# Performance work log

Hardware: AMD Instinct MI355X
Metric: run time of the kernel (lower is better)

## Reference

```python
import jax, jax.numpy as jnp
import numpy as np

N_NODES = 32000
N_EDGES = 320000
N_GRAPHS = 1600
HID = 128
RBF = 32
ZDIM = 2 * HID + RBF  # CGConv concat dim = 288


def setup_inputs() -> dict:
    key = jax.random.key(0)
    ks = jax.random.split(key, 20)
    inp = {
        "x": jax.random.randint(ks[0], (N_NODES,), 0, 100),
        "edge_index": jax.random.randint(ks[1], (2, N_EDGES), 0, N_NODES),
        "edge_attr": jax.random.normal(ks[2], (N_EDGES, RBF), dtype=jnp.float32),
        "batch": jnp.sort(jax.random.randint(ks[3], (N_NODES,), 0, N_GRAPHS)),
        "emb": jax.random.normal(ks[4], (100, HID), dtype=jnp.float32) * 0.02,
    }
    s = 1.0 / np.sqrt(ZDIM)
    for i, k0 in zip((1, 2, 3), range(5, 11, 2)):
        inp[f"Wf{i}"] = jax.random.uniform(ks[k0], (ZDIM, HID), jnp.float32, -s, s)
        inp[f"bf{i}"] = jnp.zeros((HID,), jnp.float32)
        inp[f"Ws{i}"] = jax.random.uniform(ks[k0 + 1], (ZDIM, HID), jnp.float32, -s, s)
        inp[f"bs{i}"] = jnp.zeros((HID,), jnp.float32)
    sl = 1.0 / np.sqrt(HID)
    inp["Wlin"] = jax.random.uniform(ks[11], (HID, HID), jnp.float32, -sl, sl)
    inp["blin"] = jnp.zeros((HID,), jnp.float32)
    return inp


def _cgconv(h, src, dst, ea, Wf, bf, Ws, bs):
    # PyG CGConv: z = [x_i, x_j, e_ij]; msg = sigmoid(lin_f(z)) * softplus(lin_s(z)); out = x + sum_j msg
    z = jnp.concatenate([h[dst], h[src], ea], axis=1)  # [E, 288]
    msg = jax.nn.sigmoid(z @ Wf + bf) * jax.nn.softplus(z @ Ws + bs)  # [E, 128]
    return h + jax.ops.segment_sum(msg, dst, num_segments=N_NODES)


def reference(x, edge_index, edge_attr, batch, emb,
              Wf1, bf1, Ws1, bs1, Wf2, bf2, Ws2, bs2, Wf3, bf3, Ws3, bs3,
              Wlin, blin):
    src, dst = edge_index[0], edge_index[1]
    h = emb[x]  # [N, 128] embedding lookup
    h = jax.nn.relu(_cgconv(h, src, dst, edge_attr, Wf1, bf1, Ws1, bs1))
    h = jax.nn.relu(_cgconv(h, src, dst, edge_attr, Wf2, bf2, Ws2, bs2))
    h = jax.nn.relu(_cgconv(h, src, dst, edge_attr, Wf3, bf3, Ws3, bs3))
    # global mean pool over graphs
    sums = jax.ops.segment_sum(h, batch, num_segments=N_GRAPHS)  # [G, 128]
    cnt = jax.ops.segment_sum(jnp.ones((N_NODES,), h.dtype), batch, num_segments=N_GRAPHS)
    pooled = sums / jnp.maximum(cnt, 1.0)[:, None]
    return pooled @ Wlin + blin  # [G, 128]
```

## Files before the change

### kernel.cpp

```cpp
#include <hip/hip_runtime.h>
#include <math.h>

#define NN 32000
#define NE 320000
#define NG 1600

using frag_ab = __attribute__((ext_vector_type(8))) short;
using frag_cd = __attribute__((ext_vector_type(4))) float;
typedef float v2f __attribute__((ext_vector_type(2)));

static __device__ __forceinline__ unsigned short f2bf(float f) {
  unsigned u = __builtin_bit_cast(unsigned, f);
  unsigned r = u + 0x7fff + ((u >> 16) & 1);
  return (unsigned short)(r >> 16);
}
static __device__ __forceinline__ float bflo(unsigned u) {
  return __builtin_bit_cast(float, u << 16);
}
static __device__ __forceinline__ float bfhi(unsigned u) {
  return __builtin_bit_cast(float, u & 0xffff0000u);
}
static __device__ __forceinline__ v2f unpk(unsigned u) {
  return (v2f){bflo(u), bfhi(u)};
}

__global__ __launch_bounds__(256) void k_misc(const int* __restrict__ x,
                                              const float* __restrict__ emb,
                                              const float* __restrict__ Wf1, const float* __restrict__ Ws1,
                                              const float* __restrict__ Wf2, const float* __restrict__ Ws2,
                                              const float* __restrict__ Wf3, const float* __restrict__ Ws3,
                                              float* __restrict__ h,
                                              unsigned short* __restrict__ hb,
                                              unsigned short* __restrict__ accumb,
                                              unsigned short* __restrict__ wedge,
                                              unsigned short* __restrict__ wgemm) {
  int b = blockIdx.x;
  int tid = threadIdx.x;
  if (b < 2000) {
    int idx = b * 256 + tid;
    int n = idx >> 4;
    int c8 = (idx & 15) << 3;
    const float* e = emb + (size_t)x[n] * 128 + c8;
    float4 v0 = *(const float4*)e;
    float4 v1 = *(const float4*)(e + 4);
    float* hp = h + (size_t)n * 128 + c8;
    *(float4*)hp = v0;
    *(float4*)(hp + 4) = v1;
    ushort4 p0, p1;
    p0.x = f2bf(v0.x); p0.y = f2bf(v0.y); p0.z = f2bf(v0.z); p0.w = f2bf(v0.w);
    p1.x = f2bf(v1.x); p1.y = f2bf(v1.y); p1.z = f2bf(v1.z); p1.w = f2bf(v1.w);
    unsigned short* hbp = hb + (size_t)n * 128 + c8;
    *(ushort4*)hbp = p0;
    *(ushort4*)(hbp + 4) = p1;
    *(uint4*)(accumb + (size_t)n * 128 + c8) = make_uint4(0, 0, 0, 0);
  } else if (b < 2096) {
    int idx = (b - 2000) * 256 + tid;
    int l = idx >> 13;
    int r = idx & 8191;
    int cc = r >> 5;
    int k = r & 31;
    int w = cc >> 6, t = (cc >> 4) & 3, c = cc & 15;
    const float* Wf = (l == 0) ? Wf1 : (l == 1) ? Wf2 : Wf3;
    const float* Ws = (l == 0) ? Ws1 : (l == 1) ? Ws2 : Ws3;
    const float* W = (t < 2) ? Wf : Ws;
    int ch = w * 32 + 2 * c + (t & 1);
    wedge[(size_t)l * 8192 + cc * 32 + k] = f2bf(W[(size_t)(256 + k) * 128 + ch]);
  } else {
    int idx = (b - 2096) * 256 + tid;
    int l = idx >> 16;
    int r = idx & 65535;
    int cc = r >> 7;
    int k = r & 127;
    int p = (cc & ~31) + ((cc & 15) << 1) + ((cc >> 4) & 1);
    int ph = p & 255;
    int j = ph >> 2, sub = ph & 3;
    const float* Wf = (l == 0) ? Wf1 : (l == 1) ? Wf2 : Wf3;
    const float* Ws = (l == 0) ? Ws1 : (l == 1) ? Ws2 : Ws3;
    const float* W = (sub < 2) ? Wf : Ws;
    int ch = 2 * j + (sub & 1);
    int krow = ((p < 256) ? 0 : 128) + k;
    wgemm[(size_t)l * 65536 + cc * 128 + k] = f2bf(W[(size_t)krow * 128 + ch]);
  }
}

__global__ __launch_bounds__(256) void k_histb(const int* __restrict__ ei,
                                               const int* __restrict__ batch,
                                               int* __restrict__ counts,
                                               int* __restrict__ starts) {
  int b = blockIdx.x;
  int tid = threadIdx.x;
  if (b < 1250) {
    int e = b * 256 + tid;
    atomicAdd(counts + ei[NE + e], 1);
  } else {
    int n = (b - 1250) * 256 + tid;
    if (n > NN) return;
    if (n == NN) {
      starts[NG] = NN;
      int last = batch[NN - 1];
      for (int g = last + 1; g < NG; ++g) starts[g] = NN;
    } else if (n == 0) {
      int bb = batch[0];
      for (int g = 0; g <= bb; ++g) starts[g] = 0;
    } else {
      int b0 = batch[n - 1], b1 = batch[n];
      for (int g = b0 + 1; g <= b1; ++g) starts[g] = n;
    }
  }
}

__global__ __launch_bounds__(1024) void k_scan(const int* __restrict__ counts,
                                               int* __restrict__ offs) {
  __shared__ int part[1024];
  __shared__ int carry_s;
  int t = threadIdx.x;
  if (t == 0) carry_s = 0;
  __syncthreads();
  for (int chunk = 0; chunk < 4; ++chunk) {
    int base = chunk * 8192 + t * 8;
    int4 a = make_int4(0, 0, 0, 0), bq = make_int4(0, 0, 0, 0);
    bool full = (base + 8 <= NN);
    if (full) {
      a = *(const int4*)(counts + base);
      bq = *(const int4*)(counts + base + 4);
    }
    int e1 = a.x, e2 = e1 + a.y, e3 = e2 + a.z, e4 = e3 + a.w;
    int e5 = e4 + bq.x, e6 = e5 + bq.y, e7 = e6 + bq.z;
    int run = e7 + bq.w;
    part[t] = run;
    __syncthreads();
    for (int off = 1; off < 1024; off <<= 1) {
      int v = (t >= off) ? part[t - off] : 0;
      __syncthreads();
      part[t] += v;
      __syncthreads();
    }
    int excl = carry_s + ((t == 0) ? 0 : part[t - 1]);
    if (full) {
      int4 o0 = make_int4(excl, excl + e1, excl + e2, excl + e3);
      int4 o1 = make_int4(excl + e4, excl + e5, excl + e6, excl + e7);
      *(int4*)(offs + base) = o0;
      *(int4*)(offs + base + 4) = o1;
    }
    __syncthreads();
    if (t == 0) carry_s += part[1023];
    __syncthreads();
  }
}

__global__ __launch_bounds__(256) void k_scat1(const int* __restrict__ ei,
                                               int* __restrict__ offs,
                                               int* __restrict__ perm) {
  int e = blockIdx.x * 256 + threadIdx.x;
  int d = ei[NE + e];
  int pos = atomicAdd(offs + d, 1);
  perm[pos] = e;
}

__global__ __launch_bounds__(256) void k_scat2(const int* __restrict__ ei,
                                               const float* __restrict__ ea,
                                               const int* __restrict__ perm,
                                               int* __restrict__ srcp,
                                               int* __restrict__ dstp,
                                               unsigned short* __restrict__ eab) {
  __shared__ int se[64];
  int b = blockIdx.x;
  int t = threadIdx.x;
  int base = b * 64;
  if (t < 64) {
    int e = perm[base + t];
    se[t] = e;
    srcp[base + t] = ei[e];
    dstp[base + t] = ei[NE + e];
  }
  __syncthreads();
  int x = t >> 2;
  int ck = t & 3;
  int e = se[x];
  const float* a = ea + (size_t)e * 32 + ck * 8;
  float4 v0 = *(const float4*)a;
  float4 v1 = *(const float4*)(a + 4);
  int p = (((x >> 2) & 3) << 4) | ((x >> 4) << 2) | (x & 3);
  unsigned short* q = eab + (size_t)(base + p) * 32 + ck * 8;
  ushort4 o0, o1;
  o0.x = f2bf(v0.x); o0.y = f2bf(v0.y); o0.z = f2bf(v0.z); o0.w = f2bf(v0.w);
  o1.x = f2bf(v1.x); o1.y = f2bf(v1.y); o1.z = f2bf(v1.z); o1.w = f2bf(v1.w);
  *(ushort4*)q = o0;
  *(ushort4*)(q + 4) = o1;
}

__global__ __launch_bounds__(256) void k_gemm(const unsigned short* __restrict__ hb,
                                              const unsigned short* __restrict__ wgemmL,
                                              unsigned short* __restrict__ T) {
  __shared__ short sA[64 * 136];
  __shared__ short sB[128 * 136];
  int m0 = blockIdx.x * 64;
  int n0 = blockIdx.y * 128;
  int tid = threadIdx.x;
#pragma unroll
  for (int i = 0; i < 4; ++i) {
    int idx = tid + i * 256;
    int row = idx >> 4, chk = idx & 15;
    uint4 v = *(const uint4*)(hb + (size_t)(m0 + row) * 128 + chk * 8);
    *(uint4*)&sA[row * 136 + chk * 8] = v;
  }
#pragma unroll
  for (int i = 0; i < 8; ++i) {
    int idx = tid + i * 256;
    int col = idx >> 4, chk = idx & 15;
    uint4 v = *(const uint4*)(wgemmL + (size_t)(n0 + col) * 128 + chk * 8);
    *(uint4*)&sB[col * 136 + chk * 8] = v;
  }
  __syncthreads();
  int w = tid >> 6, lane = tid & 63, c = lane & 15, q = lane >> 4;
  frag_cd acc[4][2];
#pragma unroll
  for (int mt = 0; mt < 4; ++mt)
#pragma unroll
    for (int t = 0; t < 2; ++t) acc[mt][t] = (frag_cd){0.f, 0.f, 0.f, 0.f};
#pragma unroll
  for (int ks = 0; ks < 4; ++ks) {
    frag_ab Af[4], Bf[2];
#pragma unroll
    for (int mt = 0; mt < 4; ++mt)
      Af[mt] = *(const frag_ab*)&sA[(mt * 16 + c) * 136 + ks * 32 + q * 8];
#pragma unroll
    for (int t = 0; t < 2; ++t)
      Bf[t] = *(const frag_ab*)&sB[(w * 32 + t * 16 + c) * 136 + ks * 32 + q * 8];
#pragma unroll
    for (int mt = 0; mt < 4; ++mt)
#pragma unroll
      for (int t = 0; t < 2; ++t)
        acc[mt][t] = __builtin_amdgcn_mfma_f32_16x16x32_bf16(Af[mt], Bf[t], acc[mt][t], 0, 0, 0);
  }
  int nbase = n0 + w * 32 + 2 * c;
#pragma unroll
  for (int mt = 0; mt < 4; ++mt) {
#pragma unroll
    for (int r = 0; r < 4; ++r) {
      int node = m0 + mt * 16 + q * 4 + r;
      unsigned pk = (unsigned)f2bf(acc[mt][0][r]) | ((unsigned)f2bf(acc[mt][1][r]) << 16);
      *(unsigned*)(T + (size_t)node * 512 + nbase) = pk;
    }
  }
}

__global__ __launch_bounds__(256) void k_edge(const int* __restrict__ srcp,
                                              const int* __restrict__ dstp,
                                              const unsigned short* __restrict__ eab,
                                              const unsigned short* __restrict__ T,
                                              const unsigned short* __restrict__ wedgeL,
                                              const float* __restrict__ bf,
                                              const float* __restrict__ bs,
                                              unsigned short* __restrict__ accumb) {
  __shared__ short sA[64 * 40];
  __shared__ short sB[256 * 40];
  __shared__ float sbf[128], sbs[128];
  __shared__ int sSrc[64], sDst[64];
  int tid = threadIdx.x;
  int e0 = blockIdx.x * 64;
  {
    int row = tid >> 2, qq = tid & 3;
    uint4 v = *(const uint4*)(eab + (size_t)e0 * 32 + tid * 8);
    *(uint4*)&sA[row * 40 + qq * 8] = v;
  }
#pragma unroll
  for (int i = 0; i < 4; ++i) {
    int idx = tid + i * 256;
    int col = idx >> 2, qq = idx & 3;
    uint4 v = *(const uint4*)(wedgeL + (size_t)col * 32 + qq * 8);
    *(uint4*)&sB[col * 40 + qq * 8] = v;
  }
  if (tid < 128) {
    sbf[tid] = bf[tid];
    sbs[tid] = bs[tid];
  } else if (tid < 192) {
    sSrc[tid - 128] = srcp[e0 + tid - 128] * 512 + 256;
  } else {
    sDst[tid - 192] = dstp[e0 + tid - 192] * 512;
  }
  __syncthreads();

  int w = tid >> 6;
  int lane = tid & 63;
  int c = lane & 15;
  int q = lane >> 4;

  frag_ab Af[4], Bf[4];
#pragma unroll
  for (int et = 0; et < 4; ++et)
    Af[et] = *(const frag_ab*)&sA[(et * 16 + c) * 40 + q * 8];
#pragma unroll
  for (int t = 0; t < 4; ++t)
    Bf[t] = *(const frag_ab*)&sB[(w * 64 + t * 16 + c) * 40 + q * 8];

  frag_cd acc[4][4];
#pragma unroll
  for (int et = 0; et < 4; ++et)
#pragma unroll
    for (int t = 0; t < 4; ++t)
      acc[et][t] = (frag_cd){0.f, 0.f, 0.f, 0.f};
#pragma unroll
  for (int et = 0; et < 4; ++et)
#pragma unroll
    for (int t = 0; t < 4; ++t)
      acc[et][t] = __builtin_amdgcn_mfma_f32_16x16x32_bf16(Af[et], Bf[t], acc[et][t], 0, 0, 0);

  int ch = w * 32 + 2 * c;
  int jo = ch * 2;
  v2f bfv = {sbf[ch], sbf[ch + 1]};
  v2f bsv = {sbs[ch], sbs[ch + 1]};

  int prevd = sDst[q * 16];
  v2f av = {0.f, 0.f};
#pragma unroll
  for (int grp = 0; grp < 2; ++grp) {
    uint2 dv[8], sv[8];
#pragma unroll
    for (int i = 0; i < 8; ++i) {
      int e = q * 16 + grp * 8 + i;
      dv[i] = *(const uint2*)(T + sDst[e] + jo);
      sv[i] = *(const uint2*)(T + sSrc[e] + jo);
    }
    v2f m[8];
#pragma unroll
    for (int i = 0; i < 8; ++i) {
      int idx = grp * 8 + i;
      int et = idx >> 2, r = idx & 3;
      v2f xf = (v2f){acc[et][0][r], acc[et][1][r]} + unpk(dv[i].x) + unpk(sv[i].x) + bfv;
      v2f xs = (v2f){acc[et][2][r], acc[et][3][r]} + unpk(dv[i].y) + unpk(sv[i].y) + bsv;
      float g0 = __builtin_amdgcn_rcpf(1.f + __expf(-xf.x));
      float g1 = __builtin_amdgcn_rcpf(1.f + __expf(-xf.y));
      float sp0 = fmaxf(xs.x, 0.f) + __logf(1.f + __expf(-fabsf(xs.x)));
      float sp1 = fmaxf(xs.y, 0.f) + __logf(1.f + __expf(-fabsf(xs.y)));
      m[i] = (v2f){g0 * sp0, g1 * sp1};
    }
#pragma unroll
    for (int i = 0; i < 8; ++i) {
      int d = sDst[q * 16 + grp * 8 + i];
      if (d != prevd) {
        unsigned pk = (unsigned)f2bf(av.x) | ((unsigned)f2bf(av.y) << 16);
        unsigned short* p = accumb + (size_t)(prevd >> 2) + ch;
        asm volatile("global_atomic_pk_add_bf16 %0, %1, off" :: "v"(p), "v"(pk) : "memory");
        av = (v2f){0.f, 0.f};
        prevd = d;
      }
      av += m[i];
    }
  }
  {
    unsigned pk = (unsigned)f2bf(av.x) | ((unsigned)f2bf(av.y) << 16);
    unsigned short* p = accumb + (size_t)(prevd >> 2) + ch;
    asm volatile("global_atomic_pk_add_bf16 %0, %1, off" :: "v"(p), "v"(pk) : "memory");
  }
}

__global__ __launch_bounds__(256) void k_update(float* __restrict__ h,
                                                unsigned short* __restrict__ hb,
                                                unsigned short* __restrict__ accumb) {
  int idx = blockIdx.x * 256 + threadIdx.x;
  size_t off = (size_t)idx * 8;
  uint4 a = *(uint4*)(accumb + off);
  float4 v0 = *(float4*)(h + off);
  float4 v1 = *(float4*)(h + off + 4);
  v0.x = fmaxf(v0.x + bflo(a.x), 0.f);
  v0.y = fmaxf(v0.y + bfhi(a.x), 0.f);
  v0.z = fmaxf(v0.z + bflo(a.y), 0.f);
  v0.w = fmaxf(v0.w + bfhi(a.y), 0.f);
  v1.x = fmaxf(v1.x + bflo(a.z), 0.f);
  v1.y = fmaxf(v1.y + bfhi(a.z), 0.f);
  v1.z = fmaxf(v1.z + bflo(a.w), 0.f);
  v1.w = fmaxf(v1.w + bfhi(a.w), 0.f);
  *(float4*)(h + off) = v0;
  *(float4*)(h + off + 4) = v1;
  ushort4 p0, p1;
  p0.x = f2bf(v0.x); p0.y = f2bf(v0.y); p0.z = f2bf(v0.z); p0.w = f2bf(v0.w);
  p1.x = f2bf(v1.x); p1.y = f2bf(v1.y); p1.z = f2bf(v1.z); p1.w = f2bf(v1.w);
  *(ushort4*)(hb + off) = p0;
  *(ushort4*)(hb + off + 4) = p1;
  *(uint4*)(accumb + off) = make_uint4(0, 0, 0, 0);
}

__global__ __launch_bounds__(256) void k_update3(float* __restrict__ h,
                                                 const unsigned short* __restrict__ accumb) {
  int idx = blockIdx.x * 256 + threadIdx.x;
  size_t off = (size_t)idx * 8;
  uint4 a = *(uint4*)(accumb + off);
  float4 v0 = *(float4*)(h + off);
  float4 v1 = *(float4*)(h + off + 4);
  v0.x = fmaxf(v0.x + bflo(a.x), 0.f);
  v0.y = fmaxf(v0.y + bfhi(a.x), 0.f);
  v0.z = fmaxf(v0.z + bflo(a.y), 0.f);
  v0.w = fmaxf(v0.w + bfhi(a.y), 0.f);
  v1.x = fmaxf(v1.x + bflo(a.z), 0.f);
  v1.y = fmaxf(v1.y + bfhi(a.z), 0.f);
  v1.z = fmaxf(v1.z + bflo(a.w), 0.f);
  v1.w = fmaxf(v1.w + bfhi(a.w), 0.f);
  *(float4*)(h + off) = v0;
  *(float4*)(h + off + 4) = v1;
}

__global__ __launch_bounds__(128) void k_pool_final(const float* __restrict__ h,
                                                    const int* __restrict__ starts,
                                                    const float* __restrict__ Wlin,
                                                    const float* __restrict__ blin,
                                                    float* __restrict__ out) {
  __shared__ float p[128];
  int g = blockIdx.x, c = threadIdx.x;
  int s0 = starts[g], s1 = starts[g + 1];
  float acc = 0.f;
  for (int n = s0; n < s1; ++n) acc += h[(size_t)n * 128 + c];
  float inv = 1.f / fmaxf((float)(s1 - s0), 1.f);
  p[c] = acc * inv;
  __syncthreads();
  float o = blin[c];
#pragma unroll 8
  for (int k = 0; k < 128; ++k) o += p[k] * Wlin[k * 128 + c];
  out[(size_t)g * 128 + c] = o;
}

extern "C" void kernel_launch(void* const* d_in, const int* in_sizes, int n_in,
                              void* d_out, int out_size, void* d_ws, size_t ws_size,
                              hipStream_t stream) {
  const int* x = (const int*)d_in[0];
  const int* ei = (const int*)d_in[1];
  const float* ea = (const float*)d_in[2];
  const int* batch = (const int*)d_in[3];
  const float* emb = (const float*)d_in[4];
  const float* Wf[3] = {(const float*)d_in[5], (const float*)d_in[9], (const float*)d_in[13]};
  const float* bf[3] = {(const float*)d_in[6], (const float*)d_in[10], (const float*)d_in[14]};
  const float* Wsm[3] = {(const float*)d_in[7], (const float*)d_in[11], (const float*)d_in[15]};
  const float* bs[3] = {(const float*)d_in[8], (const float*)d_in[12], (const float*)d_in[16]};
  const float* Wlin = (const float*)d_in[17];
  const float* blin = (const float*)d_in[18];
  float* out = (float*)d_out;

  char* ws = (char*)d_ws;
  float* h = (float*)ws;                        ws += (size_t)NN * 128 * 4;
  unsigned short* hb = (unsigned short*)ws;     ws += (size_t)NN * 128 * 2;
  unsigned short* accumb = (unsigned short*)ws; ws += (size_t)NN * 128 * 2;
  unsigned short* T = (unsigned short*)ws;      ws += (size_t)NN * 512 * 2;
  unsigned short* eab = (unsigned short*)ws;    ws += (size_t)NE * 32 * 2;
  unsigned short* wedge = (unsigned short*)ws;  ws += 3 * 8192 * 2;
  unsigned short* wgemm = (unsigned short*)ws;  ws += 3 * 65536 * 2;
  int* counts = (int*)ws;                       ws += (size_t)NN * 4;
  int* offs = (int*)ws;                         ws += (size_t)NN * 4;
  int* srcp = (int*)ws;                         ws += (size_t)NE * 4;
  int* dstp = (int*)ws;                         ws += (size_t)NE * 4;
  int* perm = (int*)ws;                         ws += (size_t)NE * 4;
  int* starts = (int*)ws;                       ws += (size_t)(NG + 1) * 4;

  hipMemsetAsync(counts, 0, (size_t)NN * 4, stream);
  k_misc<<<2864, 256, 0, stream>>>(x, emb, Wf[0], Wsm[0], Wf[1], Wsm[1], Wf[2], Wsm[2],
                                   h, hb, accumb, wedge, wgemm);
  k_histb<<<1376, 256, 0, stream>>>(ei, batch, counts, starts);
  k_scan<<<1, 1024, 0, stream>>>(counts, offs);
  k_scat1<<<1250, 256, 0, stream>>>(ei, offs, perm);
  k_scat2<<<5000, 256, 0, stream>>>(ei, ea, perm, srcp, dstp, eab);
  for (int l = 0; l < 3; ++l) {
    k_gemm<<<dim3(500, 4), 256, 0, stream>>>(hb, wgemm + (size_t)l * 65536, T);
    k_edge<<<5000, 256, 0, stream>>>(srcp, dstp, eab, T, wedge + (size_t)l * 8192,
                                     bf[l], bs[l], accumb);
    if (l < 2)
      k_update<<<2000, 256, 0, stream>>>(h, hb, accumb);
    else
      k_update3<<<2000, 256, 0, stream>>>(h, accumb);
  }
  k_pool_final<<<1600, 128, 0, stream>>>(h, starts, Wlin, blin, out);
}
```

Measured before the change: 396.6 us.

## Fuse first GEMM into scatter kernel, drop fp32 h, use exp2/log2 activations

Merges the layer-1 node GEMM with the edge-attribute scatter into one launch, and drops the fp32 hidden-state buffer so updates keep h only in bf16. Folds the last layer's ReLU update into the pooling kernel and pre-scales weights and biases by log2e so the activations can use exp2/log2, rescaling messages by ln2. This removes a kernel launch, the fp32 h traffic and some transcendental overhead. The trade-off is extra bf16 rounding of the residual state across layers.

```diff
diff --git a/kernel.cpp b/kernel.cpp
--- a/kernel.cpp
+++ b/kernel.cpp
@@ -4,6 +4,8 @@
 #define NN 32000
 #define NE 320000
 #define NG 1600
+#define LOG2E 1.4426950408889634f
+#define LN2   0.6931471805599453f
 
 using frag_ab = __attribute__((ext_vector_type(8))) short;
 using frag_cd = __attribute__((ext_vector_type(4))) float;
@@ -19,6 +21,9 @@
 }
 static __device__ __forceinline__ float bfhi(unsigned u) {
   return __builtin_bit_cast(float, u & 0xffff0000u);
+}
+static __device__ __forceinline__ float bfs(unsigned short u) {
+  return __builtin_bit_cast(float, (unsigned)u << 16);
 }
 static __device__ __forceinline__ v2f unpk(unsigned u) {
   return (v2f){bflo(u), bfhi(u)};
@@ -29,7 +34,6 @@
                                               const float* __restrict__ Wf1, const float* __restrict__ Ws1,
                                               const float* __restrict__ Wf2, const float* __restrict__ Ws2,
                                               const float* __restrict__ Wf3, const float* __restrict__ Ws3,
-                                              float* __restrict__ h,
                                               unsigned short* __restrict__ hb,
                                               unsigned short* __restrict__ accumb,
                                               unsigned short* __restrict__ wedge,
@@ -43,9 +47,6 @@
     const float* e = emb + (size_t)x[n] * 128 + c8;
     float4 v0 = *(const float4*)e;
     float4 v1 = *(const float4*)(e + 4);
-    float* hp = h + (size_t)n * 128 + c8;
-    *(float4*)hp = v0;
-    *(float4*)(hp + 4) = v1;
     ushort4 p0, p1;
     p0.x = f2bf(v0.x); p0.y = f2bf(v0.y); p0.z = f2bf(v0.z); p0.w = f2bf(v0.w);
     p1.x = f2bf(v1.x); p1.y = f2bf(v1.y); p1.z = f2bf(v1.z); p1.w = f2bf(v1.w);
@@ -64,7 +65,7 @@
     const float* Ws = (l == 0) ? Ws1 : (l == 1) ? Ws2 : Ws3;
     const float* W = (t < 2) ? Wf : Ws;
     int ch = w * 32 + 2 * c + (t & 1);
-    wedge[(size_t)l * 8192 + cc * 32 + k] = f2bf(W[(size_t)(256 + k) * 128 + ch]);
+    wedge[(size_t)l * 8192 + cc * 32 + k] = f2bf(W[(size_t)(256 + k) * 128 + ch] * LOG2E);
   } else {
     int idx = (b - 2096) * 256 + tid;
     int l = idx >> 16;
@@ -79,7 +80,7 @@
     const float* W = (sub < 2) ? Wf : Ws;
     int ch = 2 * j + (sub & 1);
     int krow = ((p < 256) ? 0 : 128) + k;
-    wgemm[(size_t)l * 65536 + cc * 128 + k] = f2bf(W[(size_t)krow * 128 + ch]);
+    wgemm[(size_t)l * 65536 + cc * 128 + k] = f2bf(W[(size_t)krow * 128 + ch] * LOG2E);
   }
 }
 
@@ -157,36 +158,92 @@
   perm[pos] = e;
 }
 
-__global__ __launch_bounds__(256) void k_scat2(const int* __restrict__ ei,
-                                               const float* __restrict__ ea,
-                                               const int* __restrict__ perm,
-                                               int* __restrict__ srcp,
-                                               int* __restrict__ dstp,
-                                               unsigned short* __restrict__ eab) {
+__global__ __launch_bounds__(256) void k_s2g(const unsigned short* __restrict__ hb,
+                                             const unsigned short* __restrict__ wgemmL,
+                                             unsigned short* __restrict__ T,
+                                             const int* __restrict__ ei,
+                                             const float* __restrict__ ea,
+                                             const int* __restrict__ perm,
+                                             int* __restrict__ srcp,
+                                             int* __restrict__ dstp,
+                                             unsigned short* __restrict__ eab) {
+  __shared__ short sA[64 * 136];
+  __shared__ short sB[128 * 136];
   __shared__ int se[64];
   int b = blockIdx.x;
-  int t = threadIdx.x;
-  int base = b * 64;
-  if (t < 64) {
-    int e = perm[base + t];
-    se[t] = e;
-    srcp[base + t] = ei[e];
-    dstp[base + t] = ei[NE + e];
-  }
-  __syncthreads();
-  int x = t >> 2;
-  int ck = t & 3;
-  int e = se[x];
-  const float* a = ea + (size_t)e * 32 + ck * 8;
-  float4 v0 = *(const float4*)a;
-  float4 v1 = *(const float4*)(a + 4);
-  int p = (((x >> 2) & 3) << 4) | ((x >> 4) << 2) | (x & 3);
-  unsigned short* q = eab + (size_t)(base + p) * 32 + ck * 8;
-  ushort4 o0, o1;
-  o0.x = f2bf(v0.x); o0.y = f2bf(v0.y); o0.z = f2bf(v0.z); o0.w = f2bf(v0.w);
-  o1.x = f2bf(v1.x); o1.y = f2bf(v1.y); o1.z = f2bf(v1.z); o1.w = f2bf(v1.w);
-  *(ushort4*)q = o0;
-  *(ushort4*)(q + 4) = o1;
+  int tid = threadIdx.x;
+  if (b < 2000) {
+    int m0 = (b >> 2) * 64;
+    int n0 = (b & 3) * 128;
+#pragma unroll
+    for (int i = 0; i < 4; ++i) {
+      int idx = tid + i * 256;
+      int row = idx >> 4, chk = idx & 15;
+      uint4 v = *(const uint4*)(hb + (size_t)(m0 + row) * 128 + chk * 8);
+      *(uint4*)&sA[row * 136 + chk * 8] = v;
+    }
+#pragma unroll
+    for (int i = 0; i < 8; ++i) {
+      int idx = tid + i * 256;
+      int col = idx >> 4, chk = idx & 15;
+      uint4 v = *(const uint4*)(wgemmL + (size_t)(n0 + col) * 128 + chk * 8);
+      *(uint4*)&sB[col * 136 + chk * 8] = v;
+    }
+    __syncthreads();
+    int w = tid >> 6, lane = tid & 63, c = lane & 15, q = lane >> 4;
+    frag_cd acc[4][2];
+#pragma unroll
+    for (int mt = 0; mt < 4; ++mt)
+#pragma unroll
+      for (int t = 0; t < 2; ++t) acc[mt][t] = (frag_cd){0.f, 0.f, 0.f, 0.f};
+#pragma unroll
+    for (int ks = 0; ks < 4; ++ks) {
+      frag_ab Af[4], Bf[2];
+#pragma unroll
+      for (int mt = 0; mt < 4; ++mt)
+        Af[mt] = *(const frag_ab*)&sA[(mt * 16 + c) * 136 + ks * 32 + q * 8];
+#pragma unroll
+      for (int t = 0; t < 2; ++t)
+        Bf[t] = *(const frag_ab*)&sB[(w * 32 + t * 16 + c) * 136 + ks * 32 + q * 8];
+#pragma unroll
+      for (int mt = 0; mt < 4; ++mt)
+#pragma unroll
+        for (int t = 0; t < 2; ++t)
+          acc[mt][t] = __builtin_amdgcn_mfma_f32_16x16x32_bf16(Af[mt], Bf[t], acc[mt][t], 0, 0, 0);
+    }
+    int nbase = n0 + w * 32 + 2 * c;
+#pragma unroll
+    for (int mt = 0; mt < 4; ++mt) {
+#pragma unroll
+      for (int r = 0; r < 4; ++r) {
+        int node = m0 + mt * 16 + q * 4 + r;
+        unsigned pk = (unsigned)f2bf(acc[mt][0][r]) | ((unsigned)f2bf(acc[mt][1][r]) << 16);
+        *(unsigned*)(T + (size_t)node * 512 + nbase) = pk;
+      }
+    }
+  } else {
+    int base = (b - 2000) * 64;
+    if (tid < 64) {
+      int e = perm[base + tid];
+      se[tid] = e;
+      srcp[base + tid] = ei[e];
+      dstp[base + tid] = ei[NE + e];
+    }
+    __syncthreads();
+    int x = tid >> 2;
+    int ck = tid & 3;
+    int e = se[x];
+    const float* a = ea + (size_t)e * 32 + ck * 8;
+    float4 v0 = *(const float4*)a;
+    float4 v1 = *(const float4*)(a + 4);
+    int p = (((x >> 2) & 3) << 4) | ((x >> 4) << 2) | (x & 3);
+    unsigned short* q = eab + (size_t)(base + p) * 32 + ck * 8;
+    ushort4 o0, o1;
+    o0.x = f2bf(v0.x); o0.y = f2bf(v0.y); o0.z = f2bf(v0.z); o0.w = f2bf(v0.w);
+    o1.x = f2bf(v1.x); o1.y = f2bf(v1.y); o1.z = f2bf(v1.z); o1.w = f2bf(v1.w);
+    *(ushort4*)q = o0;
+    *(ushort4*)(q + 4) = o1;
+  }
 }
 
 __global__ __launch_bounds__(256) void k_gemm(const unsigned short* __restrict__ hb,
@@ -272,8 +329,8 @@
     *(uint4*)&sB[col * 40 + qq * 8] = v;
   }
   if (tid < 128) {
-    sbf[tid] = bf[tid];
-    sbs[tid] = bs[tid];
+    sbf[tid] = bf[tid] * LOG2E;
+    sbs[tid] = bs[tid] * LOG2E;
   } else if (tid < 192) {
     sSrc[tid - 128] = srcp[e0 + tid - 128] * 512 + 256;
   } else {
@@ -329,17 +386,18 @@
       int et = idx >> 2, r = idx & 3;
       v2f xf = (v2f){acc[et][0][r], acc[et][1][r]} + unpk(dv[i].x) + unpk(sv[i].x) + bfv;
       v2f xs = (v2f){acc[et][2][r], acc[et][3][r]} + unpk(dv[i].y) + unpk(sv[i].y) + bsv;
-      float g0 = __builtin_amdgcn_rcpf(1.f + __expf(-xf.x));
-      float g1 = __builtin_amdgcn_rcpf(1.f + __expf(-xf.y));
-      float sp0 = fmaxf(xs.x, 0.f) + __logf(1.f + __expf(-fabsf(xs.x)));
-      float sp1 = fmaxf(xs.y, 0.f) + __logf(1.f + __expf(-fabsf(xs.y)));
+      float g0 = __builtin_amdgcn_rcpf(1.f + exp2f(-xf.x));
+      float g1 = __builtin_amdgcn_rcpf(1.f + exp2f(-xf.y));
+      float sp0 = fmaxf(xs.x, 0.f) + log2f(1.f + exp2f(-fabsf(xs.x)));
+      float sp1 = fmaxf(xs.y, 0.f) + log2f(1.f + exp2f(-fabsf(xs.y)));
       m[i] = (v2f){g0 * sp0, g1 * sp1};
     }
 #pragma unroll
     for (int i = 0; i < 8; ++i) {
       int d = sDst[q * 16 + grp * 8 + i];
       if (d != prevd) {
-        unsigned pk = (unsigned)f2bf(av.x) | ((unsigned)f2bf(av.y) << 16);
+        v2f o = av * LN2;
+        unsigned pk = (unsigned)f2bf(o.x) | ((unsigned)f2bf(o.y) << 16);
         unsigned short* p = accumb + (size_t)(prevd >> 2) + ch;
         asm volatile("global_atomic_pk_add_bf16 %0, %1, off" :: "v"(p), "v"(pk) : "memory");
         av = (v2f){0.f, 0.f};
@@ -349,58 +407,38 @@
     }
   }
   {
-    unsigned pk = (unsigned)f2bf(av.x) | ((unsigned)f2bf(av.y) << 16);
+    v2f o = av * LN2;
+    unsigned pk = (unsigned)f2bf(o.x) | ((unsigned)f2bf(o.y) << 16);
     unsigned short* p = accumb + (size_t)(prevd >> 2) + ch;
     asm volatile("global_atomic_pk_add_bf16 %0, %1, off" :: "v"(p), "v"(pk) : "memory");
   }
 }
 
-__global__ __launch_bounds__(256) void k_update(float* __restrict__ h,
-                                                unsigned short* __restrict__ hb,
+__global__ __launch_bounds__(256) void k_update(unsigned short* __restrict__ hb,
                                                 unsigned short* __restrict__ accumb) {
   int idx = blockIdx.x * 256 + threadIdx.x;
   size_t off = (size_t)idx * 8;
   uint4 a = *(uint4*)(accumb + off);
-  float4 v0 = *(float4*)(h + off);
-  float4 v1 = *(float4*)(h + off + 4);
-  v0.x = fmaxf(v0.x + bflo(a.x), 0.f);
-  v0.y = fmaxf(v0.y + bfhi(a.x), 0.f);
-  v0.z = fmaxf(v0.z + bflo(a.y), 0.f);
-  v0.w = fmaxf(v0.w + bfhi(a.y), 0.f);
-  v1.x = fmaxf(v1.x + bflo(a.z), 0.f);
-  v1.y = fmaxf(v1.y + bfhi(a.z), 0.f);
-  v1.z = fmaxf(v1.z + bflo(a.w), 0.f);
-  v1.w = fmaxf(v1.w + bfhi(a.w), 0.f);
-  *(float4*)(h + off) = v0;
-  *(float4*)(h + off + 4) = v1;
-  ushort4 p0, p1;
-  p0.x = f2bf(v0.x); p0.y = f2bf(v0.y); p0.z = f2bf(v0.z); p0.w = f2bf(v0.w);
-  p1.x = f2bf(v1.x); p1.y = f2bf(v1.y); p1.z = f2bf(v1.z); p1.w = f2bf(v1.w);
-  *(ushort4*)(hb + off) = p0;
-  *(ushort4*)(hb + off + 4) = p1;
+  uint4 hv = *(uint4*)(hb + off);
+  float r0 = fmaxf(bflo(hv.x) + bflo(a.x), 0.f);
+  float r1 = fmaxf(bfhi(hv.x) + bfhi(a.x), 0.f);
+  float r2 = fmaxf(bflo(hv.y) + bflo(a.y), 0.f);
+  float r3 = fmaxf(bfhi(hv.y) + bfhi(a.y), 0.f);
+  float r4 = fmaxf(bflo(hv.z) + bflo(a.z), 0.f);
+  float r5 = fmaxf(bfhi(hv.z) + bfhi(a.z), 0.f);
+  float r6 = fmaxf(bflo(hv.w) + bflo(a.w), 0.f);
+  float r7 = fmaxf(bfhi(hv.w) + bfhi(a.w), 0.f);
+  uint4 o;
+  o.x = (unsigned)f2bf(r0) | ((unsigned)f2bf(r1) << 16);
+  o.y = (unsigned)f2bf(r2) | ((unsigned)f2bf(r3) << 16);
+  o.z = (unsigned)f2bf(r4) | ((unsigned)f2bf(r5) << 16);
+  o.w = (unsigned)f2bf(r6) | ((unsigned)f2bf(r7) << 16);
+  *(uint4*)(hb + off) = o;
   *(uint4*)(accumb + off) = make_uint4(0, 0, 0, 0);
 }
 
-__global__ __launch_bounds__(256) void k_update3(float* __restrict__ h,
-                                                 const unsigned short* __restrict__ accumb) {
-  int idx = blockIdx.x * 256 + threadIdx.x;
-  size_t off = (size_t)idx * 8;
-  uint4 a = *(uint4*)(accumb + off);
-  float4 v0 = *(float4*)(h + off);
-  float4 v1 = *(float4*)(h + off + 4);
-  v0.x = fmaxf(v0.x + bflo(a.x), 0.f);
-  v0.y = fmaxf(v0.y + bfhi(a.x), 0.f);
-  v0.z = fmaxf(v0.z + bflo(a.y), 0.f);
-  v0.w = fmaxf(v0.w + bfhi(a.y), 0.f);
-  v1.x = fmaxf(v1.x + bflo(a.z), 0.f);
-  v1.y = fmaxf(v1.y + bfhi(a.z), 0.f);
-  v1.z = fmaxf(v1.z + bflo(a.w), 0.f);
-  v1.w = fmaxf(v1.w + bfhi(a.w), 0.f);
-  *(float4*)(h + off) = v0;
-  *(float4*)(h + off + 4) = v1;
-}
-
-__global__ __launch_bounds__(128) void k_pool_final(const float* __restrict__ h,
+__global__ __launch_bounds__(128) void k_pool_final(const unsigned short* __restrict__ hb,
+                                                    const unsigned short* __restrict__ accumb,
                                                     const int* __restrict__ starts,
                                                     const float* __restrict__ Wlin,
                                                     const float* __restrict__ blin,
@@ -409,7 +447,11 @@
   int g = blockIdx.x, c = threadIdx.x;
   int s0 = starts[g], s1 = starts[g + 1];
   float acc = 0.f;
-  for (int n = s0; n < s1; ++n) acc += h[(size_t)n * 128 + c];
+  for (int n = s0; n < s1; ++n) {
+    float hv = bfs(hb[(size_t)n * 128 + c]);
+    float av = bfs(accumb[(size_t)n * 128 + c]);
+    acc += fmaxf(hv + av, 0.f);
+  }
   float inv = 1.f / fmaxf((float)(s1 - s0), 1.f);
   p[c] = acc * inv;
   __syncthreads();
@@ -436,7 +478,6 @@
   float* out = (float*)d_out;
 
   char* ws = (char*)d_ws;
-  float* h = (float*)ws;                        ws += (size_t)NN * 128 * 4;
   unsigned short* hb = (unsigned short*)ws;     ws += (size_t)NN * 128 * 2;
   unsigned short* accumb = (unsigned short*)ws; ws += (size_t)NN * 128 * 2;
   unsigned short* T = (unsigned short*)ws;      ws += (size_t)NN * 512 * 2;
@@ -452,19 +493,18 @@
 
   hipMemsetAsync(counts, 0, (size_t)NN * 4, stream);
   k_misc<<<2864, 256, 0, stream>>>(x, emb, Wf[0], Wsm[0], Wf[1], Wsm[1], Wf[2], Wsm[2],
-                                   h, hb, accumb, wedge, wgemm);
+                                   hb, accumb, wedge, wgemm);
   k_histb<<<1376, 256, 0, stream>>>(ei, batch, counts, starts);
   k_scan<<<1, 1024, 0, stream>>>(counts, offs);
   k_scat1<<<1250, 256, 0, stream>>>(ei, offs, perm);
-  k_scat2<<<5000, 256, 0, stream>>>(ei, ea, perm, srcp, dstp, eab);
+  k_s2g<<<7000, 256, 0, stream>>>(hb, wgemm, T, ei, ea, perm, srcp, dstp, eab);
   for (int l = 0; l < 3; ++l) {
-    k_gemm<<<dim3(500, 4), 256, 0, stream>>>(hb, wgemm + (size_t)l * 65536, T);
+    if (l > 0)
+      k_gemm<<<dim3(500, 4), 256, 0, stream>>>(hb, wgemm + (size_t)l * 65536, T);
     k_edge<<<5000, 256, 0, stream>>>(srcp, dstp, eab, T, wedge + (size_t)l * 8192,
                                      bf[l], bs[l], accumb);
     if (l < 2)
-      k_update<<<2000, 256, 0, stream>>>(h, hb, accumb);
-    else
-      k_update3<<<2000, 256, 0, stream>>>(h, accumb);
-  }
-  k_pool_final<<<1600, 128, 0, stream>>>(h, starts, Wlin, blin, out);
-}
+      k_update<<<2000, 256, 0, stream>>>(hb, accumb);
+  }
+  k_pool_final<<<1600, 128, 0, stream>>>(hb, accumb, starts, Wlin, blin, out);
+}
```

Measured after the change: 384.3 us. 1.03x faster.
